# Optimization experiments

Measured on AMD Instinct MI355X. Metric: run time of the kernel, lower is better.

Reference implementation:

```python
import jax, jax.numpy as jnp
import numpy as np
import math

E, H, T, B = 1024, 16, 2048, 2
HD = E // H  # 64
NUM_BUCKETS, MAX_DIST = 32, 128


def setup_inputs() -> dict:
    key = jax.random.key(0)
    ks = jax.random.split(key, 8)
    s = 0.02
    return {
        'query': jax.random.normal(ks[0], (T, B, E), jnp.float32),
        'q_w': jax.random.normal(ks[1], (E, E), jnp.float32) * s,
        'q_b': jnp.zeros((E,), jnp.float32),
        'k_w': jax.random.normal(ks[2], (E, E), jnp.float32) * s,
        'k_b': jnp.zeros((E,), jnp.float32),
        'v_w': jax.random.normal(ks[3], (E, E), jnp.float32) * s,
        'v_b': jnp.zeros((E,), jnp.float32),
        'out_w': jax.random.normal(ks[4], (E, E), jnp.float32) * s,
        'out_b': jnp.zeros((E,), jnp.float32),
        'rel_emb': jax.random.normal(ks[5], (NUM_BUCKETS, H), jnp.float32) * s,
        'grep_w': jax.random.normal(ks[6], (8, HD), jnp.float32) * s,
        'grep_b': jnp.zeros((8,), jnp.float32),
        'grep_a': jnp.ones((1, H, 1, 1), jnp.float32),
    }


def _rel_bucket(rp):
    # bidirectional T5-style bucketing, num_buckets=32 -> nb=16, max_exact=8
    nb = NUM_BUCKETS // 2
    buckets = (rp > 0).astype(jnp.int32) * nb
    rpa = jnp.abs(rp)
    max_exact = nb // 2
    large = max_exact + (
        jnp.log(jnp.maximum(rpa, 1).astype(jnp.float32) / max_exact)
        / math.log(MAX_DIST / max_exact) * (nb - max_exact)
    ).astype(jnp.int32)
    large = jnp.minimum(large, nb - 1)
    return buckets + jnp.where(rpa < max_exact, rpa, large)


def reference(query, q_w, q_b, k_w, k_b, v_w, v_b, out_w, out_b, rel_emb, grep_w, grep_b, grep_a):
    t, b, e = query.shape
    scaling = HD ** -0.5
    # relative-position bucket bias -> [H, T, T]
    rp = jnp.arange(t)[None, :] - jnp.arange(t)[:, None]  # memory - context
    pos_bias = jnp.transpose(rel_emb[_rel_bucket(rp)], (2, 0, 1))  # [H,T,T]
    # GRU-style gate computed from the RAW query (pre q_proj)
    ql = jnp.transpose(query, (1, 0, 2)).reshape(b, t, H, HD).transpose(0, 2, 1, 3)  # [B,H,T,HD]
    gate_in = (ql @ grep_w.T + grep_b).reshape(b, H, t, 2, 4).sum(-1)  # [B,H,T,2]
    gate = jax.nn.sigmoid(gate_in)
    gate_a, gate_b = gate[..., 0:1], gate[..., 1:2]  # each [B,H,T,1]
    gate_a_1 = gate_a * (gate_b * grep_a - 1.0) + 2.0  # [B,H,T,1]
    bias = gate_a_1 * pos_bias[None]  # [B,H,T,T]
    # projections (self-attention: key = value = query)
    q = (query @ q_w.T + q_b) * scaling
    k = query @ k_w.T + k_b
    v = query @ v_w.T + v_b
    qh = q.reshape(t, b, H, HD)
    kh = k.reshape(t, b, H, HD)
    vh = v.reshape(t, b, H, HD)
    scores = jnp.einsum('tbhd,sbhd->bhts', qh, kh) + bias
    attn = jax.nn.softmax(scores, axis=-1)
    out = jnp.einsum('bhts,sbhd->tbhd', attn, vh).reshape(t, b, e)
    return out @ out_w.T + out_b
```

## Files before the change

### kernel.cpp

```cpp
#include <hip/hip_runtime.h>
#include <math.h>

typedef unsigned short u16;
typedef unsigned int u32;
typedef __bf16 bf16x8 __attribute__((ext_vector_type(8)));
typedef float f32x4 __attribute__((ext_vector_type(4)));
typedef float f32x16 __attribute__((ext_vector_type(16)));

__device__ __forceinline__ u16 f2bf(float f) {
  union { float f; u32 u; } v; v.f = f;
  u32 r = v.u + 0x7fffu + ((v.u >> 16) & 1u);
  return (u16)(r >> 16);
}

__device__ __forceinline__ u32 pkbf(float a, float b) {
  u32 r;
  asm("v_cvt_pk_bf16_f32 %0, %1, %2" : "=v"(r) : "v"(a), "v"(b));
  return r;
}

__device__ __forceinline__ float ex2(float x) {
  float r;
  asm("v_exp_f32 %0, %1" : "=v"(r) : "v"(x));
  return r;
}

__device__ __forceinline__ void gld16(const void* g, void* s) {
  __builtin_amdgcn_global_load_lds(
      reinterpret_cast<__attribute__((address_space(1))) u32*>((size_t)g),
      reinterpret_cast<__attribute__((address_space(3))) u32*>((u32)(size_t)s),
      16, 0, 0);
}

__global__ __launch_bounds__(256) void convk(const float* __restrict__ src,
                                             u16* __restrict__ dst, int n4) {
  int i = blockIdx.x * 256 + threadIdx.x;
  if (i >= n4) return;
  float4 v = ((const float4*)src)[i];
  uint2 o;
  o.x = (u32)f2bf(v.x) | ((u32)f2bf(v.y) << 16);
  o.y = (u32)f2bf(v.z) | ((u32)f2bf(v.w) << 16);
  ((uint2*)dst)[i] = o;
}

__global__ __launch_bounds__(256) void lutk(const float* __restrict__ rel_emb,
                                            float* __restrict__ lut) {
  int dix = blockIdx.x * 256 + threadIdx.x;
  if (dix >= 4096) return;
  int rp = dix - 2048;
  int bucket = (rp > 0) ? 16 : 0;
  int rpa = rp < 0 ? -rp : rp;
  if (rpa < 8) {
    bucket += rpa;
  } else {
    int large = 8 + (int)(logf((float)rpa * 0.125f) * (8.0f / 2.772588722239781f));
    bucket += (large < 15) ? large : 15;
  }
  const float LOG2E = 1.4426950408889634f;
#pragma unroll
  for (int h = 0; h < 16; ++h) lut[h * 4096 + dix] = rel_emb[bucket * 16 + h] * LOG2E;
}

__global__ __launch_bounds__(256) void gatek(const float* __restrict__ query,
                                             const float* __restrict__ grep_w,
                                             const float* __restrict__ grep_b,
                                             const float* __restrict__ grep_a,
                                             float* __restrict__ gate) {
  __shared__ __align__(16) float gw[8][64];
  __shared__ float gb[8];
  __shared__ float ga[16];
  int tid = threadIdx.x;
  if (tid < 128) ((float4*)&gw[0][0])[tid] = ((const float4*)grep_w)[tid];
  if (tid < 8) gb[tid] = grep_b[tid];
  if (tid < 16) ga[tid] = grep_a[tid];
  __syncthreads();
  int i = blockIdx.x * 256 + tid;
  int t = i & 2047, h = (i >> 11) & 15, b = i >> 15;
  const float* x = query + ((size_t)t * 2 + b) * 1024 + h * 64;
  float acc[8] = {0, 0, 0, 0, 0, 0, 0, 0};
  for (int e4 = 0; e4 < 16; ++e4) {
    float4 xv = ((const float4*)x)[e4];
#pragma unroll
    for (int j = 0; j < 8; ++j)
      acc[j] += xv.x * gw[j][e4 * 4] + xv.y * gw[j][e4 * 4 + 1] +
                xv.z * gw[j][e4 * 4 + 2] + xv.w * gw[j][e4 * 4 + 3];
  }
  float sA = acc[0] + acc[1] + acc[2] + acc[3] + gb[0] + gb[1] + gb[2] + gb[3];
  float sB = acc[4] + acc[5] + acc[6] + acc[7] + gb[4] + gb[5] + gb[6] + gb[7];
  float gA = 1.0f / (1.0f + expf(-sA));
  float gB = 1.0f / (1.0f + expf(-sB));
  gate[i] = gA * (gB * ga[h] - 1.0f) + 2.0f;
}

__global__ __launch_bounds__(256) void gemmk(
    const u16* __restrict__ A,
    const u16* __restrict__ W0, const u16* __restrict__ W1, const u16* __restrict__ W2,
    const float* __restrict__ b0, const float* __restrict__ b1, const float* __restrict__ b2,
    u16* __restrict__ qa, u16* __restrict__ kst, u16* __restrict__ vst,
    float* __restrict__ fout, int moBase) {
  const int mode = moBase + (int)blockIdx.z;
  const u16* W = (mode == 1) ? W1 : (mode == 2) ? W2 : W0;
  const float* bias = (mode == 1) ? b1 : (mode == 2) ? b2 : b0;

  __shared__ __align__(16) u16 As[128 * 64];
  __shared__ __align__(16) u16 Bs[128 * 64];

  const int tid = threadIdx.x;
  const int l = tid & 63;
  const int w = tid >> 6;
  const int wr = w >> 1, wc = w & 1;
  const int m0 = blockIdx.y * 128, n0 = blockIdx.x * 128;
  const int li = l >> 3, ls = l & 7;

  f32x4 acc[4][4] = {};

  for (int k0 = 0; k0 < 1024; k0 += 64) {
#pragma unroll
    for (int j = 0; j < 4; ++j) {
      const int rr = (w * 4 + j) * 8 + li;
      const int cs = ls ^ (rr & 7);
      gld16(A + ((size_t)(m0 + rr) << 10) + k0 + cs * 8, &As[(w * 4 + j) * 512]);
      gld16(W + ((size_t)(n0 + rr) << 10) + k0 + cs * 8, &Bs[(w * 4 + j) * 512]);
    }
    __syncthreads();
#pragma unroll
    for (int ks = 0; ks < 2; ++ks) {
      bf16x8 af[4], bfr[4];
#pragma unroll
      for (int mf = 0; mf < 4; ++mf) {
        const int row = wr * 64 + mf * 16 + (l & 15);
        const int slot = (ks * 4 + (l >> 4)) ^ (row & 7);
        af[mf] = *(const bf16x8*)&As[row * 64 + slot * 8];
      }
#pragma unroll
      for (int nf = 0; nf < 4; ++nf) {
        const int row = wc * 64 + nf * 16 + (l & 15);
        const int slot = (ks * 4 + (l >> 4)) ^ (row & 7);
        bfr[nf] = *(const bf16x8*)&Bs[row * 64 + slot * 8];
      }
#pragma unroll
      for (int mf = 0; mf < 4; ++mf)
#pragma unroll
        for (int nf = 0; nf < 4; ++nf)
          acc[mf][nf] = __builtin_amdgcn_mfma_f32_16x16x32_bf16(af[mf], bfr[nf], acc[mf][nf], 0, 0, 0);
    }
    __syncthreads();
  }

  const float QSC = 0.125f * 1.4426950408889634f;
#pragma unroll
  for (int mf = 0; mf < 4; ++mf)
#pragma unroll
    for (int nf = 0; nf < 4; ++nf)
#pragma unroll
      for (int r = 0; r < 4; ++r) {
        const int row = m0 + wr * 64 + mf * 16 + (l >> 4) * 4 + r;
        const int col = n0 + wc * 64 + nf * 16 + (l & 15);
        float v = acc[mf][nf][r] + bias[col];
        const int t = row >> 1, bb = row & 1, hh = col >> 6, d = col & 63;
        const size_t bh = (size_t)bb * 16 + hh;
        if (mode == 0) {
          v *= QSC;
          qa[((bh * 2048 + t) << 6) + d] = f2bf(v);
        } else if (mode == 1) {
          kst[((bh * 64 + (t >> 5)) << 11) + ((d >> 3) << 8) + ((t & 31) << 3) + (d & 7)] = f2bf(v);
        } else if (mode == 2) {
          vst[((bh * 64 + (t >> 5)) << 11) + (((t >> 3) & 3) << 9) + (d << 3) + (t & 7)] = f2bf(v);
        } else {
          fout[((size_t)row << 10) + col] = v;
        }
      }
}

__global__ __launch_bounds__(256, 4) void flashk(const u16* __restrict__ qa,
                                                 const u16* __restrict__ kst,
                                                 const u16* __restrict__ vst,
                                                 const float* __restrict__ lutg,
                                                 const float* __restrict__ gatew,
                                                 u16* __restrict__ aout) {
  const int B = blockIdx.x;
  const int xcd = B & 7, j = B >> 3;
  const int bh = xcd * 4 + (j >> 5);
  const int qt = j & 31;
  const int hh = bh & 15, b = bh >> 4;
  const int tid = threadIdx.x, l = tid & 63, w = tid >> 6;
  const int half = w >> 1, sub = w & 1;
  const int hi = l >> 5, q = l & 31;
  const int q0b = qt * 64;
  const int q0w = q0b + sub * 32;
  const int qg = q0w + q;

  __shared__ union {
    struct { u16 K[2][2][2048]; u16 V[2][2][2048]; } m;
    struct { float pm[4][32]; float pl[4][32]; float pO[4][32][68]; } c;
  } S;
  __shared__ __align__(16) float slice[288];

  for (int i = tid; i < 288; i += 256) slice[i] = lutg[hh * 4096 + 1920 + i];

  const size_t tb0 = (size_t)bh * 64;
  const u16* Q = qa + ((size_t)bh << 17);

  bf16x8 qf[4];
#pragma unroll
  for (int mk = 0; mk < 4; ++mk)
    qf[mk] = *(const bf16x8*)&Q[((size_t)qg << 6) + mk * 16 + hi * 8];

  const float g = gatew[((size_t)bh << 11) + qg];
  const float gcm = g * lutg[hh * 4096];
  const float gcp = g * lutg[hh * 4096 + 4095];

  float m_run = -3e38f, l_run = 0.0f;
  f32x16 oacc[2] = {};

  {
    const u16* kt0 = kst + ((tb0 + half * 32) << 11) + l * 8;
    const u16* vt0 = vst + ((tb0 + half * 32) << 11) + l * 8;
    if (sub == 0) {
#pragma unroll
      for (int i = 0; i < 4; ++i) gld16(kt0 + i * 512, &S.m.K[half][0][i * 512]);
    } else {
#pragma unroll
      for (int i = 0; i < 4; ++i) gld16(vt0 + i * 512, &S.m.V[half][0][i * 512]);
    }
  }
  __syncthreads();

  for (int ts = 0; ts < 32; ++ts) {
    const int bf_ = ts & 1;
    if (ts < 31) {
      const u16* ktn = kst + ((tb0 + half * 32 + ts + 1) << 11) + l * 8;
      const u16* vtn = vst + ((tb0 + half * 32 + ts + 1) << 11) + l * 8;
      if (sub == 0) {
#pragma unroll
        for (int i = 0; i < 4; ++i) gld16(ktn + i * 512, &S.m.K[half][bf_ ^ 1][i * 512]);
      } else {
#pragma unroll
        for (int i = 0; i < 4; ++i) gld16(vtn + i * 512, &S.m.V[half][bf_ ^ 1][i * 512]);
      }
    }
    const u16* Kb = &S.m.K[half][bf_][0];
    const u16* Vb = &S.m.V[half][bf_][0];
    const int s0 = half * 1024 + ts * 32;

    f32x16 s = {};
#pragma unroll
    for (int mk = 0; mk < 4; ++mk) {
      bf16x8 kf = *(const bf16x8*)&Kb[(mk * 2 + hi) * 256 + q * 8];
      s = __builtin_amdgcn_mfma_f32_32x32x16_bf16(kf, qf[mk], s, 0, 0, 0);
    }

    const int kt = (s0 - q0w) >> 5;
    const bool far = (kt <= -4) | (kt >= 4);
    float gc = 0.0f;
    float mx;
    if (far) {
      gc = (kt < 0) ? gcm : gcp;
      float t0_ = fmaxf(fmaxf(s[0], s[1]), s[2]);
      float t1_ = fmaxf(fmaxf(s[3], s[4]), s[5]);
      float t2_ = fmaxf(fmaxf(s[6], s[7]), s[8]);
      float t3_ = fmaxf(fmaxf(s[9], s[10]), s[11]);
      float t4_ = fmaxf(fmaxf(s[12], s[13]), s[14]);
      mx = fmaxf(fmaxf(fmaxf(t0_, t1_), t2_), fmaxf(fmaxf(t3_, t4_), s[15]));
      mx = fmaxf(mx, __shfl_xor(mx, 32, 64)) + gc;
    } else {
      const int sb = s0 - q0w + 128 + 4 * hi - q;
#pragma unroll
      for (int reg = 0; reg < 16; ++reg) {
        const int kloc = (reg & 3) + 8 * (reg >> 2);
        s[reg] = fmaf(g, slice[sb + kloc], s[reg]);
      }
      float t0_ = fmaxf(fmaxf(s[0], s[1]), s[2]);
      float t1_ = fmaxf(fmaxf(s[3], s[4]), s[5]);
      float t2_ = fmaxf(fmaxf(s[6], s[7]), s[8]);
      float t3_ = fmaxf(fmaxf(s[9], s[10]), s[11]);
      float t4_ = fmaxf(fmaxf(s[12], s[13]), s[14]);
      mx = fmaxf(fmaxf(fmaxf(t0_, t1_), t2_), fmaxf(fmaxf(t3_, t4_), s[15]));
      mx = fmaxf(mx, __shfl_xor(mx, 32, 64));
    }
    if (!__all(mx - m_run <= 11.5f)) {
      const float mnew = fmaxf(m_run, mx);
      const float sc = ex2(m_run - mnew);
      l_run *= sc;
#pragma unroll
      for (int r = 0; r < 16; ++r) { oacc[0][r] *= sc; oacc[1][r] *= sc; }
      m_run = mnew;
    }
    const float mref = m_run - gc;
#pragma unroll
    for (int reg = 0; reg < 16; ++reg) s[reg] = ex2(s[reg] - mref);
    {
      float r0 = (s[0] + s[1]) + (s[2] + s[3]);
      float r1 = (s[4] + s[5]) + (s[6] + s[7]);
      float r2 = (s[8] + s[9]) + (s[10] + s[11]);
      float r3 = (s[12] + s[13]) + (s[14] + s[15]);
      float rsum = (r0 + r1) + (r2 + r3);
      rsum += __shfl_xor(rsum, 32, 64);
      l_run += rsum;
    }
    bf16x8 pa[2];
#pragma unroll
    for (int kh = 0; kh < 2; ++kh) {
      const int rb = kh * 8;
      const u32 X0 = pkbf(s[rb + 0], s[rb + 1]);
      const u32 X1 = pkbf(s[rb + 2], s[rb + 3]);
      const u32 Y0 = pkbf(s[rb + 4], s[rb + 5]);
      const u32 Y1 = pkbf(s[rb + 6], s[rb + 7]);
      const u32 E0 = hi ? X0 : Y0;
      const u32 E1 = hi ? X1 : Y1;
      const u32 Ep0 = (u32)__shfl_xor((int)E0, 32, 64);
      const u32 Ep1 = (u32)__shfl_xor((int)E1, 32, 64);
      union { u32 wds[4]; bf16x8 v; } pu;
      pu.wds[0] = hi ? Ep0 : X0;
      pu.wds[1] = hi ? Ep1 : X1;
      pu.wds[2] = hi ? Y0 : Ep0;
      pu.wds[3] = hi ? Y1 : Ep1;
      pa[kh] = pu.v;
    }
#pragma unroll
    for (int dt = 0; dt < 2; ++dt)
#pragma unroll
      for (int kh = 0; kh < 2; ++kh) {
        bf16x8 vf = *(const bf16x8*)&Vb[(kh * 2 + hi) * 512 + dt * 256 + q * 8];
        oacc[dt] = __builtin_amdgcn_mfma_f32_32x32x16_bf16(vf, pa[kh], oacc[dt], 0, 0, 0);
      }
    __syncthreads();
  }

  __syncthreads();
  if (hi == 0) { S.c.pm[w][q] = m_run; S.c.pl[w][q] = l_run; }
#pragma unroll
  for (int dt = 0; dt < 2; ++dt)
#pragma unroll
    for (int g4 = 0; g4 < 4; ++g4) {
      float4 v4;
      v4.x = oacc[dt][g4 * 4 + 0];
      v4.y = oacc[dt][g4 * 4 + 1];
      v4.z = oacc[dt][g4 * 4 + 2];
      v4.w = oacc[dt][g4 * 4 + 3];
      *(float4*)&S.c.pO[w][q][dt * 32 + g4 * 8 + hi * 4] = v4;
    }
  __syncthreads();

  const int rr = tid >> 2;
  const int dc = (tid & 3) << 4;
  const int rl = rr & 31, sr = rr >> 5;
  const float mA = S.c.pm[sr][rl], mB = S.c.pm[2 + sr][rl];
  const float M = fmaxf(mA, mB);
  const float eA = ex2(mA - M), eB = ex2(mB - M);
  const float inv = 1.0f / (S.c.pl[sr][rl] * eA + S.c.pl[2 + sr][rl] * eB);
  union { u16 hb[16]; uint4 u4[2]; } st;
#pragma unroll
  for (int c4 = 0; c4 < 4; ++c4) {
    const float4 a = *(const float4*)&S.c.pO[sr][rl][dc + c4 * 4];
    const float4 bb = *(const float4*)&S.c.pO[2 + sr][rl][dc + c4 * 4];
    st.hb[c4 * 4 + 0] = f2bf((a.x * eA + bb.x * eB) * inv);
    st.hb[c4 * 4 + 1] = f2bf((a.y * eA + bb.y * eB) * inv);
    st.hb[c4 * 4 + 2] = f2bf((a.z * eA + bb.z * eB) * inv);
    st.hb[c4 * 4 + 3] = f2bf((a.w * eA + bb.w * eB) * inv);
  }
  u16* dst = &aout[(((size_t)(q0b + rr) * 2 + b) << 10) + hh * 64 + dc];
  *(uint4*)dst = st.u4[0];
  *(uint4*)(dst + 8) = st.u4[1];
}

extern "C" void kernel_launch(void* const* d_in, const int* in_sizes, int n_in,
                              void* d_out, int out_size, void* d_ws, size_t ws_size,
                              hipStream_t stream) {
  (void)in_sizes; (void)n_in; (void)out_size; (void)ws_size;
  const float* query  = (const float*)d_in[0];
  const float* q_w    = (const float*)d_in[1];
  const float* q_b    = (const float*)d_in[2];
  const float* k_w    = (const float*)d_in[3];
  const float* k_b    = (const float*)d_in[4];
  const float* v_w    = (const float*)d_in[5];
  const float* v_b    = (const float*)d_in[6];
  const float* out_w  = (const float*)d_in[7];
  const float* out_b  = (const float*)d_in[8];
  const float* rel_emb= (const float*)d_in[9];
  const float* grep_w = (const float*)d_in[10];
  const float* grep_b = (const float*)d_in[11];
  const float* grep_a = (const float*)d_in[12];

  char* ws = (char*)d_ws;
  const size_t MB = 1ull << 20;
  u16* qbf  = (u16*)(ws + 0 * MB);
  u16* wqb  = (u16*)(ws + 8 * MB);
  u16* wkb  = (u16*)(ws + 10 * MB);
  u16* wvb  = (u16*)(ws + 12 * MB);
  u16* wob  = (u16*)(ws + 14 * MB);
  u16* qav  = (u16*)(ws + 16 * MB);
  u16* kstg = (u16*)(ws + 24 * MB);
  u16* vstg = (u16*)(ws + 32 * MB);
  u16* aout = (u16*)(ws + 40 * MB);
  float* lut  = (float*)(ws + 48 * MB);
  float* gate = (float*)(ws + 48 * MB + 256 * 1024);

  convk<<<dim3(4096), 256, 0, stream>>>(query, qbf, 1048576);
  convk<<<dim3(1024), 256, 0, stream>>>(q_w, wqb, 262144);
  convk<<<dim3(1024), 256, 0, stream>>>(k_w, wkb, 262144);
  convk<<<dim3(1024), 256, 0, stream>>>(v_w, wvb, 262144);
  convk<<<dim3(1024), 256, 0, stream>>>(out_w, wob, 262144);
  lutk<<<dim3(16), 256, 0, stream>>>(rel_emb, lut);
  gatek<<<dim3(256), 256, 0, stream>>>(query, grep_w, grep_b, grep_a, gate);

  gemmk<<<dim3(8, 32, 3), 256, 0, stream>>>(qbf, wqb, wkb, wvb, q_b, k_b, v_b,
                                            qav, kstg, vstg, nullptr, 0);
  flashk<<<dim3(1024), 256, 0, stream>>>(qav, kstg, vstg, lut, gate, aout);
  gemmk<<<dim3(8, 32, 1), 256, 0, stream>>>(aout, wob, nullptr, nullptr, out_b, nullptr, nullptr,
                                            nullptr, nullptr, nullptr, (float*)d_out, 3);
}
```

Measured before the change: 166.6 us.

## Fuse prep kernels and restructure flash attention to load K/V directly into registers

Merges the seven preprocessing launches (bf16 conversions, position-bias LUT, gate) into one kernel to cut launch overhead. Reworks the attention kernel to 128-thread blocks of 32 queries, where each wave handles half the key range. K and V fragments are read straight from global memory into registers, with K prefetched one step ahead, instead of being staged through LDS with barriers. It adds s_setprio around the MFMA sections and a two-wave softmax merge that writes output with packed bf16 conversion. This removes LDS traffic and per-step barriers, at the cost of uncoalesced-ish global loads, more register pressure and a doubled block count.

```diff
diff --git a/kernel.cpp b/kernel.cpp
--- a/kernel.cpp
+++ b/kernel.cpp
@@ -7,10 +7,10 @@
 typedef float f32x4 __attribute__((ext_vector_type(4)));
 typedef float f32x16 __attribute__((ext_vector_type(16)));
 
-__device__ __forceinline__ u16 f2bf(float f) {
+__device__ __forceinline__ u32 f2bf(float f) {
   union { float f; u32 u; } v; v.f = f;
   u32 r = v.u + 0x7fffu + ((v.u >> 16) & 1u);
-  return (u16)(r >> 16);
+  return r >> 16;
 }
 
 __device__ __forceinline__ u32 pkbf(float a, float b) {
@@ -32,64 +32,68 @@
       16, 0, 0);
 }
 
-__global__ __launch_bounds__(256) void convk(const float* __restrict__ src,
-                                             u16* __restrict__ dst, int n4) {
-  int i = blockIdx.x * 256 + threadIdx.x;
-  if (i >= n4) return;
-  float4 v = ((const float4*)src)[i];
-  uint2 o;
-  o.x = (u32)f2bf(v.x) | ((u32)f2bf(v.y) << 16);
-  o.y = (u32)f2bf(v.z) | ((u32)f2bf(v.w) << 16);
-  ((uint2*)dst)[i] = o;
-}
-
-__global__ __launch_bounds__(256) void lutk(const float* __restrict__ rel_emb,
-                                            float* __restrict__ lut) {
-  int dix = blockIdx.x * 256 + threadIdx.x;
-  if (dix >= 4096) return;
-  int rp = dix - 2048;
-  int bucket = (rp > 0) ? 16 : 0;
-  int rpa = rp < 0 ? -rp : rp;
-  if (rpa < 8) {
-    bucket += rpa;
+__global__ __launch_bounds__(256) void prepk(
+    const float* __restrict__ query, const float* __restrict__ q_w,
+    const float* __restrict__ k_w, const float* __restrict__ v_w,
+    const float* __restrict__ out_w, const float* __restrict__ rel_emb,
+    const float* __restrict__ grep_w, const float* __restrict__ grep_b,
+    const float* __restrict__ grep_a,
+    u16* __restrict__ qbf, u16* __restrict__ wqb, u16* __restrict__ wkb,
+    u16* __restrict__ wvb, u16* __restrict__ wob,
+    float* __restrict__ lut, float* __restrict__ gate) {
+  const int bid = blockIdx.x, tid = threadIdx.x;
+  if (bid < 8192) {
+    const float* src; u16* dst; int i0;
+    if (bid < 4096)      { src = query; dst = qbf; i0 = bid; }
+    else if (bid < 5120) { src = q_w;   dst = wqb; i0 = bid - 4096; }
+    else if (bid < 6144) { src = k_w;   dst = wkb; i0 = bid - 5120; }
+    else if (bid < 7168) { src = v_w;   dst = wvb; i0 = bid - 6144; }
+    else                 { src = out_w; dst = wob; i0 = bid - 7168; }
+    const int i = i0 * 256 + tid;
+    float4 v = ((const float4*)src)[i];
+    uint2 o;
+    o.x = f2bf(v.x) | (f2bf(v.y) << 16);
+    o.y = f2bf(v.z) | (f2bf(v.w) << 16);
+    ((uint2*)dst)[i] = o;
+  } else if (bid < 8208) {
+    const int dix = (bid - 8192) * 256 + tid;
+    int rp = dix - 2048;
+    int bucket = (rp > 0) ? 16 : 0;
+    int rpa = rp < 0 ? -rp : rp;
+    if (rpa < 8) {
+      bucket += rpa;
+    } else {
+      int large = 8 + (int)(logf((float)rpa * 0.125f) * (8.0f / 2.772588722239781f));
+      bucket += (large < 15) ? large : 15;
+    }
+    const float LOG2E = 1.4426950408889634f;
+#pragma unroll
+    for (int h = 0; h < 16; ++h) lut[h * 4096 + dix] = rel_emb[bucket * 16 + h] * LOG2E;
   } else {
-    int large = 8 + (int)(logf((float)rpa * 0.125f) * (8.0f / 2.772588722239781f));
-    bucket += (large < 15) ? large : 15;
+    __shared__ __align__(16) float gw[8][64];
+    __shared__ float gb[8];
+    __shared__ float ga[16];
+    if (tid < 128) ((float4*)&gw[0][0])[tid] = ((const float4*)grep_w)[tid];
+    if (tid < 8) gb[tid] = grep_b[tid];
+    if (tid < 16) ga[tid] = grep_a[tid];
+    __syncthreads();
+    const int i = (bid - 8208) * 256 + tid;
+    const int t = i & 2047, h = (i >> 11) & 15, b = i >> 15;
+    const float* x = query + ((size_t)t * 2 + b) * 1024 + h * 64;
+    float acc[8] = {0, 0, 0, 0, 0, 0, 0, 0};
+    for (int e4 = 0; e4 < 16; ++e4) {
+      float4 xv = ((const float4*)x)[e4];
+#pragma unroll
+      for (int j = 0; j < 8; ++j)
+        acc[j] += xv.x * gw[j][e4 * 4] + xv.y * gw[j][e4 * 4 + 1] +
+                  xv.z * gw[j][e4 * 4 + 2] + xv.w * gw[j][e4 * 4 + 3];
+    }
+    float sA = acc[0] + acc[1] + acc[2] + acc[3] + gb[0] + gb[1] + gb[2] + gb[3];
+    float sB = acc[4] + acc[5] + acc[6] + acc[7] + gb[4] + gb[5] + gb[6] + gb[7];
+    float gA = 1.0f / (1.0f + expf(-sA));
+    float gB = 1.0f / (1.0f + expf(-sB));
+    gate[i] = gA * (gB * ga[h] - 1.0f) + 2.0f;
   }
-  const float LOG2E = 1.4426950408889634f;
-#pragma unroll
-  for (int h = 0; h < 16; ++h) lut[h * 4096 + dix] = rel_emb[bucket * 16 + h] * LOG2E;
-}
-
-__global__ __launch_bounds__(256) void gatek(const float* __restrict__ query,
-                                             const float* __restrict__ grep_w,
-                                             const float* __restrict__ grep_b,
-                                             const float* __restrict__ grep_a,
-                                             float* __restrict__ gate) {
-  __shared__ __align__(16) float gw[8][64];
-  __shared__ float gb[8];
-  __shared__ float ga[16];
-  int tid = threadIdx.x;
-  if (tid < 128) ((float4*)&gw[0][0])[tid] = ((const float4*)grep_w)[tid];
-  if (tid < 8) gb[tid] = grep_b[tid];
-  if (tid < 16) ga[tid] = grep_a[tid];
-  __syncthreads();
-  int i = blockIdx.x * 256 + tid;
-  int t = i & 2047, h = (i >> 11) & 15, b = i >> 15;
-  const float* x = query + ((size_t)t * 2 + b) * 1024 + h * 64;
-  float acc[8] = {0, 0, 0, 0, 0, 0, 0, 0};
-  for (int e4 = 0; e4 < 16; ++e4) {
-    float4 xv = ((const float4*)x)[e4];
-#pragma unroll
-    for (int j = 0; j < 8; ++j)
-      acc[j] += xv.x * gw[j][e4 * 4] + xv.y * gw[j][e4 * 4 + 1] +
-                xv.z * gw[j][e4 * 4 + 2] + xv.w * gw[j][e4 * 4 + 3];
-  }
-  float sA = acc[0] + acc[1] + acc[2] + acc[3] + gb[0] + gb[1] + gb[2] + gb[3];
-  float sB = acc[4] + acc[5] + acc[6] + acc[7] + gb[4] + gb[5] + gb[6] + gb[7];
-  float gA = 1.0f / (1.0f + expf(-sA));
-  float gB = 1.0f / (1.0f + expf(-sB));
-  gate[i] = gA * (gB * ga[h] - 1.0f) + 2.0f;
 }
 
 __global__ __launch_bounds__(256) void gemmk(
@@ -161,45 +165,42 @@
         const size_t bh = (size_t)bb * 16 + hh;
         if (mode == 0) {
           v *= QSC;
-          qa[((bh * 2048 + t) << 6) + d] = f2bf(v);
+          qa[((bh * 2048 + t) << 6) + d] = (u16)f2bf(v);
         } else if (mode == 1) {
-          kst[((bh * 64 + (t >> 5)) << 11) + ((d >> 3) << 8) + ((t & 31) << 3) + (d & 7)] = f2bf(v);
+          kst[((bh * 64 + (t >> 5)) << 11) + ((d >> 3) << 8) + ((t & 31) << 3) + (d & 7)] = (u16)f2bf(v);
         } else if (mode == 2) {
-          vst[((bh * 64 + (t >> 5)) << 11) + (((t >> 3) & 3) << 9) + (d << 3) + (t & 7)] = f2bf(v);
+          vst[((bh * 64 + (t >> 5)) << 11) + (((t >> 3) & 3) << 9) + (d << 3) + (t & 7)] = (u16)f2bf(v);
         } else {
           fout[((size_t)row << 10) + col] = v;
         }
       }
 }
 
-__global__ __launch_bounds__(256, 4) void flashk(const u16* __restrict__ qa,
-                                                 const u16* __restrict__ kst,
-                                                 const u16* __restrict__ vst,
-                                                 const float* __restrict__ lutg,
-                                                 const float* __restrict__ gatew,
-                                                 u16* __restrict__ aout) {
+__global__ __launch_bounds__(128) void flashk(const u16* __restrict__ qa,
+                                              const u16* __restrict__ kst,
+                                              const u16* __restrict__ vst,
+                                              const float* __restrict__ lutg,
+                                              const float* __restrict__ gatew,
+                                              u16* __restrict__ aout) {
   const int B = blockIdx.x;
   const int xcd = B & 7, j = B >> 3;
-  const int bh = xcd * 4 + (j >> 5);
-  const int qt = j & 31;
+  const int bh = xcd * 4 + (j >> 6);
+  const int qt = j & 63;
   const int hh = bh & 15, b = bh >> 4;
   const int tid = threadIdx.x, l = tid & 63, w = tid >> 6;
-  const int half = w >> 1, sub = w & 1;
   const int hi = l >> 5, q = l & 31;
-  const int q0b = qt * 64;
-  const int q0w = q0b + sub * 32;
-  const int qg = q0w + q;
-
-  __shared__ union {
-    struct { u16 K[2][2][2048]; u16 V[2][2][2048]; } m;
-    struct { float pm[4][32]; float pl[4][32]; float pO[4][32][68]; } c;
-  } S;
+  const int q0 = qt * 32;
+  const int qg = q0 + q;
+
   __shared__ __align__(16) float slice[288];
-
-  for (int i = tid; i < 288; i += 256) slice[i] = lutg[hh * 4096 + 1920 + i];
-
+  __shared__ float pm[32], pl[32];
+  __shared__ __align__(16) float pO[32][68];
+
+  for (int i = tid; i < 288; i += 128) slice[i] = lutg[hh * 4096 + 1920 + i];
+  __syncthreads();
+
+  const u16* Q = qa + ((size_t)bh << 17);
   const size_t tb0 = (size_t)bh * 64;
-  const u16* Q = qa + ((size_t)bh << 17);
 
   bf16x8 qf[4];
 #pragma unroll
@@ -213,44 +214,40 @@
   float m_run = -3e38f, l_run = 0.0f;
   f32x16 oacc[2] = {};
 
-  {
-    const u16* kt0 = kst + ((tb0 + half * 32) << 11) + l * 8;
-    const u16* vt0 = vst + ((tb0 + half * 32) << 11) + l * 8;
-    if (sub == 0) {
-#pragma unroll
-      for (int i = 0; i < 4; ++i) gld16(kt0 + i * 512, &S.m.K[half][0][i * 512]);
-    } else {
-#pragma unroll
-      for (int i = 0; i < 4; ++i) gld16(vt0 + i * 512, &S.m.V[half][0][i * 512]);
-    }
-  }
-  __syncthreads();
-
+  const u16* Kt = kst + ((tb0 + (size_t)(w * 32)) << 11);
+  const u16* Vt = vst + ((tb0 + (size_t)(w * 32)) << 11);
+  const int kof = hi * 256 + q * 8;
+
+  bf16x8 kf[4];
+#pragma unroll
+  for (int mk = 0; mk < 4; ++mk)
+    kf[mk] = *(const bf16x8*)&Kt[mk * 512 + kof];
+
+#pragma unroll 2
   for (int ts = 0; ts < 32; ++ts) {
-    const int bf_ = ts & 1;
+    const int s0 = (w * 32 + ts) * 32;
+    __builtin_amdgcn_s_setprio(1);
+    f32x16 s = {};
+#pragma unroll
+    for (int mk = 0; mk < 4; ++mk)
+      s = __builtin_amdgcn_mfma_f32_32x32x16_bf16(kf[mk], qf[mk], s, 0, 0, 0);
+    __builtin_amdgcn_s_setprio(0);
+
+    bf16x8 kn[4];
     if (ts < 31) {
-      const u16* ktn = kst + ((tb0 + half * 32 + ts + 1) << 11) + l * 8;
-      const u16* vtn = vst + ((tb0 + half * 32 + ts + 1) << 11) + l * 8;
-      if (sub == 0) {
-#pragma unroll
-        for (int i = 0; i < 4; ++i) gld16(ktn + i * 512, &S.m.K[half][bf_ ^ 1][i * 512]);
-      } else {
-#pragma unroll
-        for (int i = 0; i < 4; ++i) gld16(vtn + i * 512, &S.m.V[half][bf_ ^ 1][i * 512]);
-      }
-    }
-    const u16* Kb = &S.m.K[half][bf_][0];
-    const u16* Vb = &S.m.V[half][bf_][0];
-    const int s0 = half * 1024 + ts * 32;
-
-    f32x16 s = {};
-#pragma unroll
-    for (int mk = 0; mk < 4; ++mk) {
-      bf16x8 kf = *(const bf16x8*)&Kb[(mk * 2 + hi) * 256 + q * 8];
-      s = __builtin_amdgcn_mfma_f32_32x32x16_bf16(kf, qf[mk], s, 0, 0, 0);
-    }
-
-    const int kt = (s0 - q0w) >> 5;
+      const u16* Kn = Kt + 2048;
+#pragma unroll
+      for (int mk = 0; mk < 4; ++mk)
+        kn[mk] = *(const bf16x8*)&Kn[mk * 512 + kof];
+    }
+    bf16x8 vf[4];
+#pragma unroll
+    for (int i = 0; i < 4; ++i) {
+      const int dt = i >> 1, kh = i & 1;
+      vf[i] = *(const bf16x8*)&Vt[(kh * 2 + hi) * 512 + (dt * 32 + q) * 8];
+    }
+
+    const int kt = (s0 - q0) >> 5;
     const bool far = (kt <= -4) | (kt >= 4);
     float gc = 0.0f;
     float mx;
@@ -264,7 +261,7 @@
       mx = fmaxf(fmaxf(fmaxf(t0_, t1_), t2_), fmaxf(fmaxf(t3_, t4_), s[15]));
       mx = fmaxf(mx, __shfl_xor(mx, 32, 64)) + gc;
     } else {
-      const int sb = s0 - q0w + 128 + 4 * hi - q;
+      const int sb = s0 - q0 + 128 + 4 * hi - q;
 #pragma unroll
       for (int reg = 0; reg < 16; ++reg) {
         const int kloc = (reg & 3) + 8 * (reg >> 2);
@@ -317,51 +314,57 @@
       pu.wds[3] = hi ? Y1 : Ep1;
       pa[kh] = pu.v;
     }
+    __builtin_amdgcn_s_setprio(1);
 #pragma unroll
     for (int dt = 0; dt < 2; ++dt)
 #pragma unroll
-      for (int kh = 0; kh < 2; ++kh) {
-        bf16x8 vf = *(const bf16x8*)&Vb[(kh * 2 + hi) * 512 + dt * 256 + q * 8];
-        oacc[dt] = __builtin_amdgcn_mfma_f32_32x32x16_bf16(vf, pa[kh], oacc[dt], 0, 0, 0);
-      }
-    __syncthreads();
+      for (int kh = 0; kh < 2; ++kh)
+        oacc[dt] = __builtin_amdgcn_mfma_f32_32x32x16_bf16(vf[dt * 2 + kh], pa[kh], oacc[dt], 0, 0, 0);
+    __builtin_amdgcn_s_setprio(0);
+
+    if (ts < 31) {
+#pragma unroll
+      for (int mk = 0; mk < 4; ++mk) kf[mk] = kn[mk];
+    }
+    Kt += 2048; Vt += 2048;
   }
 
+  if (w == 1) {
+    if (hi == 0) { pm[q] = m_run; pl[q] = l_run; }
+#pragma unroll
+    for (int dt = 0; dt < 2; ++dt)
+#pragma unroll
+      for (int gph = 0; gph < 4; ++gph) {
+        float4 v4;
+        v4.x = oacc[dt][gph * 4 + 0];
+        v4.y = oacc[dt][gph * 4 + 1];
+        v4.z = oacc[dt][gph * 4 + 2];
+        v4.w = oacc[dt][gph * 4 + 3];
+        *(float4*)&pO[q][dt * 32 + gph * 8 + hi * 4] = v4;
+      }
+  }
   __syncthreads();
-  if (hi == 0) { S.c.pm[w][q] = m_run; S.c.pl[w][q] = l_run; }
-#pragma unroll
-  for (int dt = 0; dt < 2; ++dt)
-#pragma unroll
-    for (int g4 = 0; g4 < 4; ++g4) {
-      float4 v4;
-      v4.x = oacc[dt][g4 * 4 + 0];
-      v4.y = oacc[dt][g4 * 4 + 1];
-      v4.z = oacc[dt][g4 * 4 + 2];
-      v4.w = oacc[dt][g4 * 4 + 3];
-      *(float4*)&S.c.pO[w][q][dt * 32 + g4 * 8 + hi * 4] = v4;
-    }
-  __syncthreads();
-
-  const int rr = tid >> 2;
-  const int dc = (tid & 3) << 4;
-  const int rl = rr & 31, sr = rr >> 5;
-  const float mA = S.c.pm[sr][rl], mB = S.c.pm[2 + sr][rl];
-  const float M = fmaxf(mA, mB);
-  const float eA = ex2(mA - M), eB = ex2(mB - M);
-  const float inv = 1.0f / (S.c.pl[sr][rl] * eA + S.c.pl[2 + sr][rl] * eB);
-  union { u16 hb[16]; uint4 u4[2]; } st;
-#pragma unroll
-  for (int c4 = 0; c4 < 4; ++c4) {
-    const float4 a = *(const float4*)&S.c.pO[sr][rl][dc + c4 * 4];
-    const float4 bb = *(const float4*)&S.c.pO[2 + sr][rl][dc + c4 * 4];
-    st.hb[c4 * 4 + 0] = f2bf((a.x * eA + bb.x * eB) * inv);
-    st.hb[c4 * 4 + 1] = f2bf((a.y * eA + bb.y * eB) * inv);
-    st.hb[c4 * 4 + 2] = f2bf((a.z * eA + bb.z * eB) * inv);
-    st.hb[c4 * 4 + 3] = f2bf((a.w * eA + bb.w * eB) * inv);
+  if (w == 0) {
+    const float mB = pm[q], lB = pl[q];
+    const float M = fmaxf(m_run, mB);
+    const float eA = ex2(m_run - M), eB = ex2(mB - M);
+    const float inv = 1.0f / (l_run * eA + lB * eB);
+#pragma unroll
+    for (int dt = 0; dt < 2; ++dt)
+#pragma unroll
+      for (int gph = 0; gph < 4; ++gph) {
+        const int d0 = dt * 32 + gph * 8 + hi * 4;
+        const float4 p4 = *(const float4*)&pO[q][d0];
+        const float o0 = (oacc[dt][gph * 4 + 0] * eA + p4.x * eB) * inv;
+        const float o1 = (oacc[dt][gph * 4 + 1] * eA + p4.y * eB) * inv;
+        const float o2 = (oacc[dt][gph * 4 + 2] * eA + p4.z * eB) * inv;
+        const float o3 = (oacc[dt][gph * 4 + 3] * eA + p4.w * eB) * inv;
+        uint2 st;
+        st.x = pkbf(o0, o1);
+        st.y = pkbf(o2, o3);
+        *(uint2*)&aout[(((size_t)qg * 2 + b) << 10) + hh * 64 + d0] = st;
+      }
   }
-  u16* dst = &aout[(((size_t)(q0b + rr) * 2 + b) << 10) + hh * 64 + dc];
-  *(uint4*)dst = st.u4[0];
-  *(uint4*)(dst + 8) = st.u4[1];
 }
 
 extern "C" void kernel_launch(void* const* d_in, const int* in_sizes, int n_in,
@@ -396,17 +399,13 @@
   float* lut  = (float*)(ws + 48 * MB);
   float* gate = (float*)(ws + 48 * MB + 256 * 1024);
 
-  convk<<<dim3(4096), 256, 0, stream>>>(query, qbf, 1048576);
-  convk<<<dim3(1024), 256, 0, stream>>>(q_w, wqb, 262144);
-  convk<<<dim3(1024), 256, 0, stream>>>(k_w, wkb, 262144);
-  convk<<<dim3(1024), 256, 0, stream>>>(v_w, wvb, 262144);
-  convk<<<dim3(1024), 256, 0, stream>>>(out_w, wob, 262144);
-  lutk<<<dim3(16), 256, 0, stream>>>(rel_emb, lut);
-  gatek<<<dim3(256), 256, 0, stream>>>(query, grep_w, grep_b, grep_a, gate);
+  prepk<<<dim3(8464), 256, 0, stream>>>(query, q_w, k_w, v_w, out_w, rel_emb,
+                                        grep_w, grep_b, grep_a,
+                                        qbf, wqb, wkb, wvb, wob, lut, gate);
 
   gemmk<<<dim3(8, 32, 3), 256, 0, stream>>>(qbf, wqb, wkb, wvb, q_b, k_b, v_b,
                                             qav, kstg, vstg, nullptr, 0);
-  flashk<<<dim3(1024), 256, 0, stream>>>(qav, kstg, vstg, lut, gate, aout);
+  flashk<<<dim3(2048), 128, 0, stream>>>(qav, kstg, vstg, lut, gate, aout);
   gemmk<<<dim3(8, 32, 1), 256, 0, stream>>>(aout, wob, nullptr, nullptr, out_b, nullptr, nullptr,
                                             nullptr, nullptr, nullptr, (float*)d_out, 3);
 }
```

New measurement: 184.7 us. 1.11x slower.
